# Kernel optimization log

Measured on AMD Instinct MI355X. Metric: run time of the kernel, lower is better.

Reference implementation:

```python
import jax, jax.numpy as jnp
import numpy as np

NPOINT = 1024
RADIUS = 1.0
NSAMPLE = 32
IN_CH = 64
COOR = 3


def _fps(xyz, npoint):
    # xyz: (B, N, 3) -> (B, npoint) farthest-point-sample indices.
    # Deterministic start at index 0 (torch version starts at a random index;
    # the algorithm/math is otherwise identical).
    B, N, _ = xyz.shape

    def step(carry, _):
        distance, farthest = carry
        centroid = jnp.take_along_axis(xyz, farthest[:, None, None], axis=1)  # (B,1,3)
        d = jnp.sum((xyz - centroid) ** 2, axis=-1)  # squared dist, (B,N)
        distance = jnp.minimum(distance, d)
        nxt = jnp.argmax(distance, axis=-1)
        return (distance, nxt), farthest

    init = (jnp.full((B, N), 1e10, dtype=xyz.dtype), jnp.zeros((B,), dtype=jnp.int32))
    _, idxs = jax.lax.scan(step, init, None, length=npoint)  # (npoint, B)
    return idxs.T  # (B, npoint)


def _sqdist(src, dst):
    # (B,M,C),(B,N,C) -> (B,M,N) squared distances
    return (jnp.sum(src ** 2, -1)[:, :, None]
            - 2.0 * jnp.einsum('bmc,bnc->bmn', src, dst)
            + jnp.sum(dst ** 2, -1)[:, None, :])


def _gather(points, idx):
    # points: (B,N,C); idx: (B,S) or (B,S,G)
    if idx.ndim == 2:
        return jnp.take_along_axis(points, idx[:, :, None], axis=1)
    return jax.vmap(lambda p, i: p[i])(points, idx)


def setup_inputs() -> dict:
    key = jax.random.key(0)
    k1, k2, k3 = jax.random.split(key, 3)
    B, N = 16, 8192
    points_coor = jax.random.normal(k1, (B, COOR, N), dtype=jnp.float32)
    points_fea = jax.random.normal(k2, (B, IN_CH, N), dtype=jnp.float32)
    # Conv2d(in_channel+coor_dim -> 2*in_channel, 1x1, bias=False) weight
    W = jax.random.normal(k3, (2 * IN_CH, IN_CH + COOR), dtype=jnp.float32) * 0.05
    return {"points_coor": points_coor, "points_fea": points_fea, "W": W}


def reference(points_coor, points_fea, W):
    xyz = jnp.transpose(points_coor, (0, 2, 1))  # (B,N,3)
    fea = jnp.transpose(points_fea, (0, 2, 1))   # (B,N,C)
    B, N, _ = xyz.shape

    # S: farthest point sampling
    fps_idx = _fps(xyz, NPOINT)          # (B,S)
    new_coor = _gather(xyz, fps_idx)     # (B,S,3)

    # G: hybrid KNN / ball query
    d = _sqdist(new_coor, xyz)                       # (B,S,N)
    neg_d, group_idx = jax.lax.top_k(-d, NSAMPLE)    # smallest distances
    dvals = -neg_d                                   # (B,S,G)
    group_idx = jnp.where(dvals > RADIUS ** 2, group_idx[:, :, :1], group_idx)

    grouped_coor = _gather(xyz, group_idx)                       # (B,S,G,3)
    grouped_coor = (grouped_coor - new_coor[:, :, None, :]) / RADIUS
    grouped_fea = _gather(fea, group_idx)                        # (B,S,G,C)
    grouped = jnp.concatenate([grouped_fea, grouped_coor], axis=-1)  # (B,S,G,C+3)

    # P: 1x1 conv (no bias, no norm — build_mlp never appends the norm) + ReLU + max-pool over group
    h = jax.nn.relu(jnp.einsum('bsgc,oc->bsgo', grouped, W))     # (B,S,G,2C)
    new_fea = jnp.max(h, axis=2)                                 # (B,S,2C)

    return (jnp.transpose(new_coor, (0, 2, 1)),    # (B,3,S)
            jnp.transpose(new_fea, (0, 2, 1)))     # (B,2C,S)
```

## Files before the change

kernel.cpp:

```cpp
#include <hip/hip_runtime.h>
#include <hip/hip_bf16.h>

#define BB 16
#define NN 8192
#define SS 1024
#define GG 32
#define SORT_R2 0xBF800000u

typedef float v2f __attribute__((ext_vector_type(2)));

__device__ __forceinline__ unsigned sortable(float f) {
    unsigned u = __float_as_uint(f);
    return u ^ ((unsigned)(((int)u) >> 31) | 0x80000000u);
}

template <int CTRL, int RM>
__device__ __forceinline__ float dpp_maxf(float v) {
    int i = __float_as_int(v);
    int p = __builtin_amdgcn_update_dpp(i, i, CTRL, RM, 0xF, false);
    return fmaxf(v, __int_as_float(p));
}

template <int CTRL, int RM>
__device__ __forceinline__ unsigned dpp_minu(unsigned v) {
    int p = __builtin_amdgcn_update_dpp((int)v, (int)v, CTRL, RM, 0xF, false);
    return min(v, (unsigned)p);
}

__device__ __forceinline__ float fmax3(float a, float b, float c) {
    return fmaxf(fmaxf(a, b), c);
}

__global__ __launch_bounds__(256) void k_pts(const float* __restrict__ coor,
                                             float4* __restrict__ pts4) {
    int i = blockIdx.x * 256 + threadIdx.x;
    int b = i >> 13, n = i & (NN - 1);
    const float* cb = coor + (long)b * 3 * NN;
    float x = cb[n], y = cb[NN + n], z = cb[2 * NN + n];
    float pn = __fadd_rn(__fadd_rn(__fmul_rn(x, x), __fmul_rn(y, y)), __fmul_rn(z, z));
    pts4[i] = make_float4(x, y, z, pn);
}

__global__ __launch_bounds__(256) void k_tr(const float* __restrict__ fea,
                                            float* __restrict__ feaT) {
    __shared__ float tile[64][65];
    int b = blockIdx.y, n0 = blockIdx.x * 64;
    int t = threadIdx.x;
    int nl = t & 63, cb = t >> 6;
#pragma unroll
    for (int i = 0; i < 16; i++) {
        int c = cb * 16 + i;
        tile[nl][c] = fea[((long)b * 64 + c) * NN + n0 + nl];
    }
    __syncthreads();
    int cl = t & 63, nb = t >> 6;
#pragma unroll
    for (int i = 0; i < 16; i++) {
        int n = nb * 16 + i;
        feaT[((long)b * NN + n0 + n) * 64 + cl] = tile[n][cl];
    }
}

__global__ __launch_bounds__(512) void k_fps(const float4* __restrict__ pts4,
                                             float4* __restrict__ qpts,
                                             float* __restrict__ out) {
#pragma clang fp contract(off)
    __shared__ float xs[NN], ys[NN], zs[NN];
    __shared__ int scur[SS];
    __shared__ __align__(16) float redv[2][8];
    __shared__ int sidx[2];
    int b = blockIdx.x;
    int t = threadIdx.x;
    const float4* P = pts4 + (long)b * NN;

    v2f px[8], py[8], pz[8], dist[8];
#pragma unroll
    for (int j = 0; j < 8; j++) {
        int p0 = t + (2 * j) * 512;
        int p1 = t + (2 * j + 1) * 512;
        float4 a = P[p0];
        float4 c = P[p1];
        px[j] = v2f{a.x, c.x};
        py[j] = v2f{a.y, c.y};
        pz[j] = v2f{a.z, c.z};
        dist[j] = v2f{1e10f, 1e10f};
        xs[p0] = a.x; ys[p0] = a.y; zs[p0] = a.z;
        xs[p1] = c.x; ys[p1] = c.y; zs[p1] = c.z;
    }
    if (t == 0) { sidx[0] = 0x7FFFFFFF; sidx[1] = 0x7FFFFFFF; }
    __syncthreads();

    int cur = 0;
    for (int s = 0; s < SS; s++) {
        int par = s & 1;
        float cx = xs[cur], cy = ys[cur], cz = zs[cur];
        if (t == 0) scur[s] = cur;
        v2f cx2 = v2f{cx, cx}, cy2 = v2f{cy, cy}, cz2 = v2f{cz, cz};
#pragma unroll
        for (int j = 0; j < 8; j++) {
            v2f dx = px[j] - cx2;
            v2f dy = py[j] - cy2;
            v2f dz = pz[j] - cz2;
            v2f xx = dx * dx;
            v2f yy = dy * dy;
            v2f zz = dz * dz;
            v2f sm = xx + yy;
            v2f d = sm + zz;
            dist[j] = __builtin_elementwise_min(dist[j], d);
        }
        v2f m01 = __builtin_elementwise_max(dist[0], dist[1]);
        v2f m23 = __builtin_elementwise_max(dist[2], dist[3]);
        v2f m45 = __builtin_elementwise_max(dist[4], dist[5]);
        v2f m67 = __builtin_elementwise_max(dist[6], dist[7]);
        v2f m03 = __builtin_elementwise_max(m01, m23);
        v2f m47 = __builtin_elementwise_max(m45, m67);
        v2f m07 = __builtin_elementwise_max(m03, m47);
        float bv = fmaxf(m07.x, m07.y);
        float wv = bv;
        wv = dpp_maxf<0x111, 0xF>(wv);
        wv = dpp_maxf<0x112, 0xF>(wv);
        wv = dpp_maxf<0x114, 0xF>(wv);
        wv = dpp_maxf<0x118, 0xF>(wv);
        wv = dpp_maxf<0x142, 0xA>(wv);
        wv = dpp_maxf<0x143, 0xC>(wv);
        if ((t & 63) == 63) redv[par][t >> 6] = wv;
        __syncthreads();
        float4 r0 = *(const float4*)redv[par];
        float4 r1 = *(const float4*)(redv[par] + 4);
        float gmax = fmaxf(fmax3(r0.x, r0.y, r0.z),
                           fmax3(r0.w, fmax3(r1.x, r1.y, r1.z), r1.w));
        if (t == 0) sidx[1 - par] = 0x7FFFFFFF;
        if (bv == gmax) {
            int jj = 16;
#pragma unroll
            for (int j = 7; j >= 0; j--) {
                jj = (dist[j].y == gmax) ? (2 * j + 1) : jj;
                jj = (dist[j].x == gmax) ? (2 * j) : jj;
            }
            atomicMin(&sidx[par], t + jj * 512);
        }
        __syncthreads();
        cur = sidx[par];
    }
    __syncthreads();

#pragma unroll
    for (int s = t; s < SS; s += 512) {
        int c = scur[s];
        float cx = xs[c], cy = ys[c], cz = zs[c];
        out[(long)b * 3 * SS + s]          = cx;
        out[(long)b * 3 * SS + SS + s]     = cy;
        out[(long)b * 3 * SS + 2 * SS + s] = cz;
        float qn = __fadd_rn(__fadd_rn(__fmul_rn(cx, cx), __fmul_rn(cy, cy)),
                             __fmul_rn(cz, cz));
        qpts[(long)b * SS + s] = make_float4(cx, cy, cz, qn);
    }
}

#define SWZ(p) ((p) ^ (((p) >> 6) & 31))
__global__ __launch_bounds__(64, 1) void k_knn_mlp(const float4* __restrict__ pts4,
                                                   const float* __restrict__ feaT,
                                                   const float4* __restrict__ qpts,
                                                   const float* __restrict__ W,
                                                   float* __restrict__ out) {
    __shared__ __align__(16) unsigned dk[NN];
    int* sidxs = (int*)(dk + 2176);
    float* grouped = (float*)dk;

    int Q = blockIdx.x;
    int b = Q >> 10, s = Q & 1023;
    int l = threadIdx.x;
    float4 q = qpts[Q];
    const float4* P = pts4 + (long)b * NN;

    unsigned u0 = 0xFFFFFFFFu, u1q = 0xFFFFFFFFu;
    int p0 = 0, p1q = 0;
#pragma unroll 16
    for (int j = 0; j < 128; j++) {
        int p = j * 64 + l;
        float4 v = P[p];
        float dot = __fadd_rn(__fadd_rn(__fmul_rn(q.x, v.x), __fmul_rn(q.y, v.y)),
                              __fmul_rn(q.z, v.z));
        float d = __fadd_rn(__fsub_rn(q.w, __fmul_rn(2.0f, dot)), v.w);
        unsigned u = sortable(d);
        dk[SWZ(p)] = u;
        bool c0 = u < u0;
        bool c1 = u < u1q;
        u1q = c1 ? (c0 ? u0 : u) : u1q;
        p1q = c1 ? (c0 ? p0 : p) : p1q;
        u0 = c0 ? u : u0;
        p0 = c0 ? p : p0;
    }
    __syncthreads();

    v2f wab[68];
    {
        const float* Wr = W + l * 67;
#pragma unroll
        for (int c = 0; c < 67; c++) {
            wab[c] = v2f{Wr[c], Wr[64 * 67 + c]};
        }
        wab[67] = v2f{0.f, 0.f};
    }

    unsigned resv = 0;
    int resp = 0, pos0 = 0;
    for (int k = 0; k < GG; k++) {
        unsigned mv = u0;
        mv = dpp_minu<0x111, 0xF>(mv);
        mv = dpp_minu<0x112, 0xF>(mv);
        mv = dpp_minu<0x114, 0xF>(mv);
        mv = dpp_minu<0x118, 0xF>(mv);
        mv = dpp_minu<0x142, 0xA>(mv);
        mv = dpp_minu<0x143, 0xC>(mv);
        unsigned wmin = (unsigned)__builtin_amdgcn_readlane((int)mv, 63);
        unsigned long long mask = __ballot(u0 == wmin);
        int wpos;
        if (__builtin_popcountll(mask) == 1) {
            int owner = __builtin_ctzll(mask);
            wpos = __builtin_amdgcn_readlane(p0, owner);
        } else {
            unsigned long long kk =
                ((unsigned long long)u0 << 32) | (unsigned)p0;
#pragma unroll
            for (int m = 1; m < 64; m <<= 1) {
                unsigned long long o = __shfl_xor(kk, m, 64);
                kk = (o < kk) ? o : kk;
            }
            wpos = (int)(kk & 0xFFFFFFFFull);
        }
        if (k == 0) pos0 = wpos;
        if (l == k) { resv = wmin; resp = wpos; }
        int own = wpos & 63;
        if (l == own) {
            dk[SWZ(wpos)] = 0xFFFFFFFFu;
            u0 = u1q; p0 = p1q;
            u1q = 0xFFFFFFFFu;
        }
        unsigned oh = (unsigned)__builtin_amdgcn_readlane((int)u0, own);
        if (oh == 0xFFFFFFFFu) {
            __syncthreads();
            int rc1 = l * 64 + own;
            int rc2 = (l + 64) * 64 + own;
            unsigned v1 = dk[SWZ(rc1)], v2 = dk[SWZ(rc2)];
            bool c = v2 < v1;
            unsigned cv = c ? v2 : v1;
            int cp = c ? rc2 : rc1;
            unsigned cm = cv;
            cm = dpp_minu<0x111, 0xF>(cm);
            cm = dpp_minu<0x112, 0xF>(cm);
            cm = dpp_minu<0x114, 0xF>(cm);
            cm = dpp_minu<0x118, 0xF>(cm);
            cm = dpp_minu<0x142, 0xA>(cm);
            cm = dpp_minu<0x143, 0xC>(cm);
            unsigned colmin = (unsigned)__builtin_amdgcn_readlane((int)cm, 63);
            unsigned long long m2 = __ballot(cv == colmin);
            int colpos;
            if (__builtin_popcountll(m2) == 1) {
                colpos = __builtin_amdgcn_readlane(cp, __builtin_ctzll(m2));
            } else {
                unsigned long long kk =
                    ((unsigned long long)cv << 32) | (unsigned)cp;
#pragma unroll
                for (int m = 1; m < 64; m <<= 1) {
                    unsigned long long o = __shfl_xor(kk, m, 64);
                    kk = (o < kk) ? o : kk;
                }
                colpos = (int)(kk & 0xFFFFFFFFull);
            }
            if (l == own) { u0 = colmin; p0 = colpos; }
        }
    }

    if (l < GG) sidxs[l] = (resv > SORT_R2) ? pos0 : resp;
    __syncthreads();

    if (l < 32) {
        int idx = sidxs[l];
        float4 p = pts4[(long)b * NN + idx];
        float4 rc = make_float4(__fsub_rn(p.x, q.x), __fsub_rn(p.y, q.y),
                                __fsub_rn(p.z, q.z), 0.f);
        *(float4*)&grouped[l * 68 + 64] = rc;
    }
    {
        int g = l >> 1, half = l & 1;
        int idx = sidxs[g];
        const float4* f4 = (const float4*)(feaT + ((long)b * NN + idx) * 64);
#pragma unroll
        for (int k4 = 0; k4 < 8; k4++) {
            *(float4*)&grouped[g * 68 + half * 32 + k4 * 4] = f4[half * 8 + k4];
        }
    }
    __syncthreads();

    v2f mm = v2f{-1e30f, -1e30f};
#pragma unroll 2
    for (int g = 0; g < GG; g++) {
        v2f a = v2f{0.f, 0.f};
#pragma unroll
        for (int c4 = 0; c4 < 17; c4++) {
            float4 gv = *(float4*)&grouped[g * 68 + c4 * 4];
            a = __builtin_elementwise_fma(v2f{gv.x, gv.x}, wab[4 * c4 + 0], a);
            a = __builtin_elementwise_fma(v2f{gv.y, gv.y}, wab[4 * c4 + 1], a);
            a = __builtin_elementwise_fma(v2f{gv.z, gv.z}, wab[4 * c4 + 2], a);
            a = __builtin_elementwise_fma(v2f{gv.w, gv.w}, wab[4 * c4 + 3], a);
        }
        mm = __builtin_elementwise_max(mm, a);
    }
    out[49152 + ((long)b * 128 + l) * SS + s]      = fmaxf(mm.x, 0.f);
    out[49152 + ((long)b * 128 + l + 64) * SS + s] = fmaxf(mm.y, 0.f);
}

extern "C" void kernel_launch(void* const* d_in, const int* in_sizes, int n_in,
                              void* d_out, int out_size, void* d_ws, size_t ws_size,
                              hipStream_t stream) {
    const float* coor = (const float*)d_in[0];
    const float* fea  = (const float*)d_in[1];
    const float* Wm   = (const float*)d_in[2];
    float* out = (float*)d_out;

    char* ws = (char*)d_ws;
    float4* pts4 = (float4*)ws;
    float*  feaT = (float*)(ws + 2097152);
    float4* qpts = (float4*)(ws + 2097152 + 33554432);

    k_pts<<<(BB * NN) / 256, 256, 0, stream>>>(coor, pts4);
    k_tr<<<dim3(NN / 64, BB), 256, 0, stream>>>(fea, feaT);
    k_fps<<<BB, 512, 0, stream>>>(pts4, qpts, out);
    k_knn_mlp<<<BB * SS, 64, 0, stream>>>(pts4, feaT, qpts, Wm, out);
}
```

Before: 1.432 ms.

## Replace LDS distance cache with recompute and per-lane consumed bitmasks in KNN

Drops the 32KB shared-memory array holding all 8192 sortable distances per query. When a lane's top-2 candidates run out, the column distances are recomputed from global point data, and already-taken points are masked using per-lane 64-bit bitmasks fetched by shuffle. This removes the LDS writes and barriers and shrinks LDS use, which should allow more 64-thread blocks per CU. In exchange, each refill now does extra global loads and distance arithmetic.

```diff
diff --git a/kernel.cpp b/kernel.cpp
--- a/kernel.cpp
+++ b/kernel.cpp
@@ -157,15 +157,13 @@
     }
 }
 
-#define SWZ(p) ((p) ^ (((p) >> 6) & 31))
 __global__ __launch_bounds__(64, 1) void k_knn_mlp(const float4* __restrict__ pts4,
                                                    const float* __restrict__ feaT,
                                                    const float4* __restrict__ qpts,
                                                    const float* __restrict__ W,
                                                    float* __restrict__ out) {
-    __shared__ __align__(16) unsigned dk[NN];
-    int* sidxs = (int*)(dk + 2176);
-    float* grouped = (float*)dk;
+    __shared__ __align__(16) float grouped[GG * 68];
+    __shared__ int sidxs[GG];
 
     int Q = blockIdx.x;
     int b = Q >> 10, s = Q & 1023;
@@ -183,7 +181,6 @@
                               __fmul_rn(q.z, v.z));
         float d = __fadd_rn(__fsub_rn(q.w, __fmul_rn(2.0f, dot)), v.w);
         unsigned u = sortable(d);
-        dk[SWZ(p)] = u;
         bool c0 = u < u0;
         bool c1 = u < u1q;
         u1q = c1 ? (c0 ? u0 : u) : u1q;
@@ -191,7 +188,6 @@
         u0 = c0 ? u : u0;
         p0 = c0 ? p : p0;
     }
-    __syncthreads();
 
     v2f wab[68];
     {
@@ -203,6 +199,7 @@
         wab[67] = v2f{0.f, 0.f};
     }
 
+    unsigned long long consLo = 0ull, consHi = 0ull;
     unsigned resv = 0;
     int resp = 0, pos0 = 0;
     for (int k = 0; k < GG; k++) {
@@ -233,18 +230,32 @@
         if (l == k) { resv = wmin; resp = wpos; }
         int own = wpos & 63;
         if (l == own) {
-            dk[SWZ(wpos)] = 0xFFFFFFFFu;
+            int jj = wpos >> 6;
+            if (jj < 64) consLo |= 1ull << jj;
+            else         consHi |= 1ull << (jj - 64);
             u0 = u1q; p0 = p1q;
             u1q = 0xFFFFFFFFu;
         }
         unsigned oh = (unsigned)__builtin_amdgcn_readlane((int)u0, own);
         if (oh == 0xFFFFFFFFu) {
-            __syncthreads();
+            unsigned long long mLo = __shfl(consLo, own, 64);
+            unsigned long long mHi = __shfl(consHi, own, 64);
             int rc1 = l * 64 + own;
             int rc2 = (l + 64) * 64 + own;
-            unsigned v1 = dk[SWZ(rc1)], v2 = dk[SWZ(rc2)];
-            bool c = v2 < v1;
-            unsigned cv = c ? v2 : v1;
+            float4 a1 = P[rc1];
+            float4 a2 = P[rc2];
+            float dot1 = __fadd_rn(__fadd_rn(__fmul_rn(q.x, a1.x), __fmul_rn(q.y, a1.y)),
+                                   __fmul_rn(q.z, a1.z));
+            float d1 = __fadd_rn(__fsub_rn(q.w, __fmul_rn(2.0f, dot1)), a1.w);
+            unsigned uu1 = sortable(d1);
+            float dot2 = __fadd_rn(__fadd_rn(__fmul_rn(q.x, a2.x), __fmul_rn(q.y, a2.y)),
+                                   __fmul_rn(q.z, a2.z));
+            float d2 = __fadd_rn(__fsub_rn(q.w, __fmul_rn(2.0f, dot2)), a2.w);
+            unsigned uu2 = sortable(d2);
+            if ((mLo >> l) & 1) uu1 = 0xFFFFFFFFu;
+            if ((mHi >> l) & 1) uu2 = 0xFFFFFFFFu;
+            bool c = uu2 < uu1;
+            unsigned cv = c ? uu2 : uu1;
             int cp = c ? rc2 : rc1;
             unsigned cm = cv;
             cm = dpp_minu<0x111, 0xF>(cm);
```

Result: faster. 1.269 ms, median of 2 (-11.4%).
